# Optimization experiments

Hardware: AMD Instinct MI355X
Metric: run time of the kernel (lower is better)

## Reference

```python
import jax, jax.numpy as jnp
import numpy as np

N, P, C = 100000, 64, 128
DIST_TH = 0.1


def setup_inputs() -> dict:
    key = jax.random.key(0)
    ks = jax.random.split(key, 12)
    xyz = jax.random.uniform(ks[0], (N, 3), jnp.float32) * 10.0  # room coords in [0,10)^3
    feature = jax.random.normal(ks[1], (N, C), jnp.float32)
    center = jax.random.uniform(ks[2], (P, 3), jnp.float32) * 10.0
    normal = jax.random.normal(ks[3], (P, 3), jnp.float32)
    normal = normal / jnp.linalg.norm(normal, axis=1, keepdims=True)
    pmin = center - 1.5  # axis-aligned extent used on axes 0,1
    pmax = center + 1.5
    inp = {
        'feature': feature, 'xyz': xyz,
        'plane_center': center, 'plane_normal': normal,
        'plane_min': pmin, 'plane_max': pmax,
        'W1': jax.random.normal(ks[4], (C, 2 * C), jnp.float32) * (1.0 / np.sqrt(C)),
        's1': jnp.ones((2 * C,), jnp.float32), 'b1': jnp.zeros((2 * C,), jnp.float32),
        'W2': jax.random.normal(ks[5], (2 * C, C), jnp.float32) * (1.0 / np.sqrt(2 * C)),
        's2': jnp.ones((C,), jnp.float32), 'b2': jnp.zeros((C,), jnp.float32),
        'W3': jax.random.normal(ks[6], (C, 1), jnp.float32) * (1.0 / np.sqrt(C)),
        'b3': jnp.zeros((1,), jnp.float32),
        'Wa': jax.random.normal(ks[7], (C, C), jnp.float32) * (1.0 / np.sqrt(C)),
        'Wm': jax.random.normal(ks[8], (C, C), jnp.float32) * (1.0 / np.sqrt(C)),
        'bm': jnp.zeros((C,), jnp.float32),
    }
    return inp


def reference(feature, xyz, plane_center, plane_normal, plane_min, plane_max,
              W1, s1, b1, W2, s2, b2, W3, b3, Wa, Wm, bm):
    # pointwise MLP (shared across planes): fc1 (conv+BN+ReLU), fc2 (conv+BN+ReLU)
    h = jax.nn.relu((feature @ W1) * s1 + b1)          # [N, 2C]
    h2 = jax.nn.relu((h @ W2) * s2 + b2)               # [N, C] == plane_feature
    logit = (h2 @ W3 + b3)[:, 0]                        # [N] fc3 logits (plane_result)

    # per-plane point membership masks (dense [N, P])
    proj = xyz @ plane_normal.T                         # [N, P]
    offs = jnp.sum(plane_center * plane_normal, axis=1) # [P]
    dist_mask = jnp.abs(proj - offs[None, :]) < DIST_TH
    rng = ((xyz[:, None, 0] >= plane_min[None, :, 0]) & (xyz[:, None, 0] < plane_max[None, :, 0]) &
           (xyz[:, None, 1] >= plane_min[None, :, 1]) & (xyz[:, None, 1] < plane_max[None, :, 1]))
    mask = dist_mask & rng                              # [N, P]

    on_sel = jax.nn.sigmoid(logit) > 0.5                # [N]
    on_mask = (mask & on_sel[:, None]).astype(feature.dtype)
    off_mask = (mask & ~on_sel[:, None]).astype(feature.dtype)

    # attention pooling: masked softmax over points, per plane, per channel
    a = h2 @ Wa                                         # [N, C] att activations
    e = jnp.exp(a - jnp.max(a, axis=0, keepdims=True))  # stable exp, [N, C]
    eh = e * h2

    def att_pool(m):                                    # m: [N, P] float
        num = jnp.einsum('np,nc->pc', m, eh)
        den = jnp.einsum('np,nc->pc', m, e)
        agg = num / (den + 1e-9)                        # masked-softmax weighted sum
        return jax.nn.relu(agg @ Wm + bm)               # att_pooling.mlp (conv+ReLU)

    ori = jnp.concatenate([plane_center, plane_normal, plane_min, plane_max], axis=1)  # [P, 12]
    on_feat = jnp.concatenate([att_pool(on_mask), ori], axis=1)    # [P, C+12]
    off_feat = jnp.concatenate([att_pool(off_mask), ori], axis=1)  # [P, C+12]
    return logit, on_feat, off_feat
```

## Files before the change

kernel.cpp:

```cpp
#include <hip/hip_runtime.h>

#define NPTS 100000
#define P 64
#define C 128
#define CHUNKS 16
#define CHUNK_PTS 6250
#define CHUNK_PAD 6400

typedef __bf16 bf16_t;
typedef __bf16 bf16x4 __attribute__((ext_vector_type(4)));
typedef __bf16 bf16x8 __attribute__((ext_vector_type(8)));
typedef float floatx4 __attribute__((ext_vector_type(4)));


__global__ __launch_bounds__(256) void prep_kernel(
    const float* __restrict__ W1, const float* __restrict__ s1,
    const float* __restrict__ W2, const float* __restrict__ s2,
    const float* __restrict__ Wa,
    bf16_t* __restrict__ W1t, bf16_t* __restrict__ W2t, bf16_t* __restrict__ Wat)
{
  int i0 = blockIdx.x * blockDim.x + threadIdx.x;
  int stride = gridDim.x * blockDim.x;
  for (int i = i0; i < 256 * 128; i += stride) {
    int n = i >> 7, k = i & 127;
    W1t[i] = (bf16_t)(W1[k * 256 + n] * s1[n]);
  }
  for (int i = i0; i < 128 * 256; i += stride) {
    int n = i >> 8, k = i & 255;
    W2t[i] = (bf16_t)(W2[k * 128 + n] * s2[n]);
  }
  for (int i = i0; i < 128 * 128; i += stride) {
    int n = i >> 7, k = i & 127;
    Wat[i] = (bf16_t)(Wa[k * 128 + n]);
  }
}

__global__ __launch_bounds__(256, 6) void main_kernel(
    const float* __restrict__ feature,
    const float* __restrict__ b1, const float* __restrict__ b2,
    const float* __restrict__ W3, const float* __restrict__ b3,
    const bf16_t* __restrict__ W1t, const bf16_t* __restrict__ W2t,
    const bf16_t* __restrict__ Wat,
    bf16_t* __restrict__ rec, float* __restrict__ out_logit)
{
  __shared__ __align__(16) char smem[8704 + 16896 + 512];
  bf16_t* A1  = (bf16_t*)smem;
  bf16_t* Hs  = (bf16_t*)(smem + 8704);
  bf16_t* aB  = (bf16_t*)(smem + 8704);
  float*  w3S = (float*)(smem + 8704 + 16896);

  const int tid  = threadIdx.x;
  const int wave = tid >> 6, lane = tid & 63;
  const int quad = lane >> 4, l16 = lane & 15;
  const int m0 = blockIdx.x * 32;

  if (tid < 128) w3S[tid] = W3[tid];

#pragma unroll
  for (int j = 0; j < 4; ++j) {
    int idx = j * 256 + tid;
    int r = idx >> 5, c4 = idx & 31;
    float4 v = *(const float4*)(feature + (size_t)(m0 + r) * C + c4 * 4);
    bf16x4 o = {(bf16_t)v.x, (bf16_t)v.y, (bf16_t)v.z, (bf16_t)v.w};
    *(bf16x4*)(A1 + r * 136 + c4 * 4) = o;
  }
  __syncthreads();

  const floatx4 zero4 = {0.f, 0.f, 0.f, 0.f};

  {
    floatx4 acc[2][4];
#pragma unroll
    for (int mt = 0; mt < 2; ++mt)
#pragma unroll
      for (int nt = 0; nt < 4; ++nt) acc[mt][nt] = zero4;
#pragma unroll
    for (int kt = 0; kt < 4; ++kt) {
      bf16x8 af[2], bf[4];
#pragma unroll
      for (int mt = 0; mt < 2; ++mt)
        af[mt] = *(const bf16x8*)(A1 + (mt * 16 + l16) * 136 + kt * 32 + quad * 8);
#pragma unroll
      for (int nt = 0; nt < 4; ++nt)
        bf[nt] = *(const bf16x8*)(W1t + (wave * 64 + nt * 16 + l16) * 128 + kt * 32 + quad * 8);
#pragma unroll
      for (int mt = 0; mt < 2; ++mt)
#pragma unroll
        for (int nt = 0; nt < 4; ++nt)
          acc[mt][nt] = __builtin_amdgcn_mfma_f32_16x16x32_bf16(af[mt], bf[nt], acc[mt][nt], 0, 0, 0);
    }
#pragma unroll
    for (int nt = 0; nt < 4; ++nt) {
      int col = wave * 64 + nt * 16 + l16;
      float bias = b1[col];
#pragma unroll
      for (int mt = 0; mt < 2; ++mt)
#pragma unroll
        for (int r = 0; r < 4; ++r) {
          float hv = fmaxf(acc[mt][nt][r] + bias, 0.f);
          Hs[(mt * 16 + quad * 4 + r) * 264 + col] = (bf16_t)hv;
        }
    }
  }
  __syncthreads();

  {
    floatx4 acc[2][2];
#pragma unroll
    for (int mt = 0; mt < 2; ++mt) { acc[mt][0] = zero4; acc[mt][1] = zero4; }
#pragma unroll
    for (int kt = 0; kt < 8; ++kt) {
      bf16x8 af[2], bf[2];
#pragma unroll
      for (int mt = 0; mt < 2; ++mt)
        af[mt] = *(const bf16x8*)(Hs + (mt * 16 + l16) * 264 + kt * 32 + quad * 8);
#pragma unroll
      for (int nt = 0; nt < 2; ++nt)
        bf[nt] = *(const bf16x8*)(W2t + (wave * 32 + nt * 16 + l16) * 256 + kt * 32 + quad * 8);
#pragma unroll
      for (int mt = 0; mt < 2; ++mt)
#pragma unroll
        for (int nt = 0; nt < 2; ++nt)
          acc[mt][nt] = __builtin_amdgcn_mfma_f32_16x16x32_bf16(af[mt], bf[nt], acc[mt][nt], 0, 0, 0);
    }
#pragma unroll
    for (int nt = 0; nt < 2; ++nt) {
      int col = wave * 32 + nt * 16 + l16;
      float bias = b2[col];
#pragma unroll
      for (int mt = 0; mt < 2; ++mt)
#pragma unroll
        for (int r = 0; r < 4; ++r) {
          float hv = fmaxf(acc[mt][nt][r] + bias, 0.f);
          A1[(mt * 16 + quad * 4 + r) * 136 + col] = (bf16_t)hv;
        }
    }
  }
  __syncthreads();

  {
    floatx4 acc[2][2];
#pragma unroll
    for (int mt = 0; mt < 2; ++mt) { acc[mt][0] = zero4; acc[mt][1] = zero4; }
#pragma unroll
    for (int kt = 0; kt < 4; ++kt) {
      bf16x8 af[2], bf[2];
#pragma unroll
      for (int mt = 0; mt < 2; ++mt)
        af[mt] = *(const bf16x8*)(A1 + (mt * 16 + l16) * 136 + kt * 32 + quad * 8);
#pragma unroll
      for (int nt = 0; nt < 2; ++nt)
        bf[nt] = *(const bf16x8*)(Wat + (wave * 32 + nt * 16 + l16) * 128 + kt * 32 + quad * 8);
#pragma unroll
      for (int mt = 0; mt < 2; ++mt)
#pragma unroll
        for (int nt = 0; nt < 2; ++nt)
          acc[mt][nt] = __builtin_amdgcn_mfma_f32_16x16x32_bf16(af[mt], bf[nt], acc[mt][nt], 0, 0, 0);
    }
#pragma unroll
    for (int nt = 0; nt < 2; ++nt) {
      int col = wave * 32 + nt * 16 + l16;
#pragma unroll
      for (int mt = 0; mt < 2; ++mt)
#pragma unroll
        for (int r = 0; r < 4; ++r)
          aB[(mt * 16 + quad * 4 + r) * 136 + col] = (bf16_t)acc[mt][nt][r];
    }
  }
  __syncthreads();

  {
    const int m = tid >> 3, g = tid & 7, c0g = g * 16;
    float lsum = 0.f;
#pragma unroll
    for (int cc = 0; cc < 2; ++cc) {
      bf16x8 v = *(const bf16x8*)(A1 + m * 136 + c0g + cc * 8);
#pragma unroll
      for (int j = 0; j < 8; ++j)
        lsum += (float)v[j] * w3S[c0g + cc * 8 + j];
    }
    lsum += __shfl_xor(lsum, 1);
    lsum += __shfl_xor(lsum, 2);
    lsum += __shfl_xor(lsum, 4);
    if (g == 0) out_logit[m0 + m] = lsum + b3[0];
  }

#pragma unroll
  for (int i = tid; i < 32 * 64; i += 256) {
    int pt = i >> 6, slot = i & 63;
    const bf16_t* src = (slot < 32) ? (aB + pt * 136 + slot * 4)
                                    : (A1 + pt * 136 + (slot - 32) * 4);
    uint2 v = *(const uint2*)src;
    *(uint2*)(rec + (size_t)(m0 + pt) * 256 + slot * 4) = v;
  }
}

__global__ __launch_bounds__(256) void pool_kernel(
    const float* __restrict__ xyz, const float* __restrict__ out_logit,
    const bf16_t* __restrict__ rec,
    const float* __restrict__ ctr, const float* __restrict__ nrm,
    const float* __restrict__ pmn, const float* __restrict__ pmx,
    float* __restrict__ partial)
{
  const int plane = blockIdx.x >> 4;
  const int chunk = blockIdx.x & 15;
  const int tid = threadIdx.x, lane = tid & 63;

  __shared__ float accS[4][128];
  for (int i = tid; i < 512; i += 256) ((float*)accS)[i] = 0.f;

  const float nx = nrm[plane * 3], ny = nrm[plane * 3 + 1], nz = nrm[plane * 3 + 2];
  const float offs = ctr[plane * 3] * nx + ctr[plane * 3 + 1] * ny + ctr[plane * 3 + 2] * nz;
  const float mnx = pmn[plane * 3], mny = pmn[plane * 3 + 1];
  const float mxx = pmx[plane * 3], mxy = pmx[plane * 3 + 1];
  __syncthreads();

  const int base = chunk * CHUNK_PTS;
  float nOn0 = 0, nOn1 = 0, dOn0 = 0, dOn1 = 0;
  float nOf0 = 0, nOf1 = 0, dOf0 = 0, dOf1 = 0;

  for (int i = tid; i < CHUNK_PAD; i += 256) {
    int pt = base + i;
    bool hit = false;
    if (i < CHUNK_PTS) {
      float x = xyz[pt * 3], y = xyz[pt * 3 + 1], z = xyz[pt * 3 + 2];
      float proj = x * nx + y * ny + z * nz;
      hit = (fabsf(proj - offs) < 0.1f) &&
            (x >= mnx) && (x < mxx) && (y >= mny) && (y < mxy);
    }
    unsigned long long m = __ballot(hit);
    while (m) {
      int l = __builtin_ctzll(m);
      m &= m - 1;
      int hpt = __shfl(pt, l);
      float lg = out_logit[hpt];
      const unsigned* r32 = (const unsigned*)(rec + (size_t)hpt * 256);
      unsigned ap = r32[lane];
      unsigned hp = r32[64 + lane];
      float a0 = __uint_as_float(ap << 16);
      float a1 = __uint_as_float(ap & 0xffff0000u);
      float h0 = __uint_as_float(hp << 16);
      float h1 = __uint_as_float(hp & 0xffff0000u);
      float e0 = __expf(a0), e1 = __expf(a1);
      if (lg > 0.f) { nOn0 += e0 * h0; nOn1 += e1 * h1; dOn0 += e0; dOn1 += e1; }
      else          { nOf0 += e0 * h0; nOf1 += e1 * h1; dOf0 += e0; dOf1 += e1; }
    }
  }

  atomicAdd(&accS[0][lane * 2],     nOn0);
  atomicAdd(&accS[0][lane * 2 + 1], nOn1);
  atomicAdd(&accS[1][lane * 2],     dOn0);
  atomicAdd(&accS[1][lane * 2 + 1], dOn1);
  atomicAdd(&accS[2][lane * 2],     nOf0);
  atomicAdd(&accS[2][lane * 2 + 1], nOf1);
  atomicAdd(&accS[3][lane * 2],     dOf0);
  atomicAdd(&accS[3][lane * 2 + 1], dOf1);
  __syncthreads();

  float* dst = partial + (size_t)blockIdx.x * 512;
  for (int i = tid; i < 512; i += 256) dst[i] = ((float*)accS)[i];
}

__global__ __launch_bounds__(256) void finalize_kernel(
    const float* __restrict__ partial,
    const float* __restrict__ Wm, const float* __restrict__ bm,
    const float* __restrict__ ctr, const float* __restrict__ nrm,
    const float* __restrict__ pmn, const float* __restrict__ pmx,
    float* __restrict__ out)
{
  int sel = blockIdx.x >> 6, p = blockIdx.x & 63;
  int tid = threadIdx.x, j = tid & 127, half = tid >> 7;
  __shared__ float numS[2][128], denS[2][128], aggS[128], sumS[2][128];

  const float* bp = partial + ((size_t)p * 16 + half * 8) * 512 + sel * 256;
  float num = 0.f, den = 0.f;
#pragma unroll
  for (int k = 0; k < 8; ++k) {
    num += bp[k * 512 + j];
    den += bp[k * 512 + 128 + j];
  }
  numS[half][j] = num;
  denS[half][j] = den;
  __syncthreads();
  if (tid < 128)
    aggS[tid] = (numS[0][tid] + numS[1][tid]) / (denS[0][tid] + denS[1][tid] + 1e-9f);
  __syncthreads();

  float s = 0.f;
  const int cbase = half * 64;
#pragma unroll 8
  for (int c = 0; c < 64; ++c)
    s += aggS[cbase + c] * Wm[(cbase + c) * C + j];
  sumS[half][j] = s;
  __syncthreads();

  float* dst = out + NPTS + sel * (P * 140) + p * 140;
  if (tid < 128)
    dst[tid] = fmaxf(sumS[0][tid] + sumS[1][tid] + bm[tid], 0.f);
  if (tid < 12) {
    float v;
    if (tid < 3)      v = ctr[p * 3 + tid];
    else if (tid < 6) v = nrm[p * 3 + tid - 3];
    else if (tid < 9) v = pmn[p * 3 + tid - 6];
    else              v = pmx[p * 3 + tid - 9];
    dst[C + tid] = v;
  }
}

extern "C" void kernel_launch(void* const* d_in, const int* in_sizes, int n_in,
                              void* d_out, int out_size, void* d_ws, size_t ws_size,
                              hipStream_t stream)
{
  const float* feature = (const float*)d_in[0];
  const float* xyz     = (const float*)d_in[1];
  const float* ctr     = (const float*)d_in[2];
  const float* nrm     = (const float*)d_in[3];
  const float* pmn     = (const float*)d_in[4];
  const float* pmx     = (const float*)d_in[5];
  const float* W1      = (const float*)d_in[6];
  const float* s1      = (const float*)d_in[7];
  const float* b1      = (const float*)d_in[8];
  const float* W2      = (const float*)d_in[9];
  const float* s2      = (const float*)d_in[10];
  const float* b2      = (const float*)d_in[11];
  const float* W3      = (const float*)d_in[12];
  const float* b3      = (const float*)d_in[13];
  const float* Wa      = (const float*)d_in[14];
  const float* Wm      = (const float*)d_in[15];
  const float* bm      = (const float*)d_in[16];
  float* out = (float*)d_out;

  char* ws = (char*)d_ws;
  bf16_t* W1t = (bf16_t*)(ws);
  bf16_t* W2t = (bf16_t*)(ws + 65536);
  bf16_t* Wat = (bf16_t*)(ws + 131072);
  bf16_t* rec = (bf16_t*)(ws + 163840);
  float* partial = (float*)(ws + 163840 + (size_t)NPTS * 512);

  prep_kernel<<<64, 256, 0, stream>>>(W1, s1, W2, s2, Wa, W1t, W2t, Wat);
  main_kernel<<<NPTS / 32, 256, 0, stream>>>(
      feature, b1, b2, W3, b3, W1t, W2t, Wat, rec, out);
  pool_kernel<<<64 * CHUNKS, 256, 0, stream>>>(
      xyz, out, rec, ctr, nrm, pmn, pmx, partial);
  finalize_kernel<<<128, 256, 0, stream>>>(partial, Wm, bm, ctr, nrm, pmn, pmx, out);
}
```

Baseline: 204.1 us.

## Restructure MLP kernel so each wave independently processes 16 points

The main MLP kernel is reorganized so that each wave owns a 16-point tile and computes all output columns itself. Feature rows go straight from global memory into MFMA A-fragments, and intermediate activations stay in a per-wave LDS region, which removes the block-wide __syncthreads barriers. Each wave now reads the full weight matrices from global/L2 memory, so weight traffic per point roughly doubles compared with the 32-point block tile. Register pressure also rises (16 accumulators, cached biases), and the occupancy hint in launch bounds is dropped.

```diff
diff --git a/kernel.cpp b/kernel.cpp
--- a/kernel.cpp
+++ b/kernel.cpp
@@ -6,9 +6,9 @@
 #define CHUNKS 16
 #define CHUNK_PTS 6250
 #define CHUNK_PAD 6400
+#define NWAVES 6250
 
 typedef __bf16 bf16_t;
-typedef __bf16 bf16x4 __attribute__((ext_vector_type(4)));
 typedef __bf16 bf16x8 __attribute__((ext_vector_type(8)));
 typedef float floatx4 __attribute__((ext_vector_type(4)));
 
@@ -35,7 +35,9 @@
   }
 }
 
-__global__ __launch_bounds__(256, 6) void main_kernel(
+#define HSTRIDE 264
+
+__global__ __launch_bounds__(256) void main_kernel(
     const float* __restrict__ feature,
     const float* __restrict__ b1, const float* __restrict__ b2,
     const float* __restrict__ W3, const float* __restrict__ b3,
@@ -43,155 +45,123 @@
     const bf16_t* __restrict__ Wat,
     bf16_t* __restrict__ rec, float* __restrict__ out_logit)
 {
-  __shared__ __align__(16) char smem[8704 + 16896 + 512];
-  bf16_t* A1  = (bf16_t*)smem;
-  bf16_t* Hs  = (bf16_t*)(smem + 8704);
-  bf16_t* aB  = (bf16_t*)(smem + 8704);
-  float*  w3S = (float*)(smem + 8704 + 16896);
+  __shared__ __align__(16) bf16_t hS[4][16 * HSTRIDE];
 
   const int tid  = threadIdx.x;
   const int wave = tid >> 6, lane = tid & 63;
-  const int quad = lane >> 4, l16 = lane & 15;
-  const int m0 = blockIdx.x * 32;
-
-  if (tid < 128) w3S[tid] = W3[tid];
-
-#pragma unroll
-  for (int j = 0; j < 4; ++j) {
-    int idx = j * 256 + tid;
-    int r = idx >> 5, c4 = idx & 31;
-    float4 v = *(const float4*)(feature + (size_t)(m0 + r) * C + c4 * 4);
-    bf16x4 o = {(bf16_t)v.x, (bf16_t)v.y, (bf16_t)v.z, (bf16_t)v.w};
-    *(bf16x4*)(A1 + r * 136 + c4 * 4) = o;
-  }
-  __syncthreads();
+  const int q = lane >> 4, l = lane & 15;
+  const int wid = blockIdx.x * 4 + wave;
+  if (wid >= NWAVES) return;
+  const int m0 = wid * 16;
+  bf16_t* hw = &hS[wave][0];
+
+  bf16x8 afeat[4];
+#pragma unroll
+  for (int kt = 0; kt < 4; ++kt) {
+    const float* src = feature + (size_t)(m0 + l) * C + kt * 32 + q * 8;
+    float4 v0 = *(const float4*)(src);
+    float4 v1 = *(const float4*)(src + 4);
+    bf16x8 o = {(bf16_t)v0.x, (bf16_t)v0.y, (bf16_t)v0.z, (bf16_t)v0.w,
+                (bf16_t)v1.x, (bf16_t)v1.y, (bf16_t)v1.z, (bf16_t)v1.w};
+    afeat[kt] = o;
+  }
+
+  float b1r[16], b2r[8];
+#pragma unroll
+  for (int nt = 0; nt < 16; ++nt) b1r[nt] = b1[nt * 16 + l];
+#pragma unroll
+  for (int nt = 0; nt < 8; ++nt)  b2r[nt] = b2[nt * 16 + l];
 
   const floatx4 zero4 = {0.f, 0.f, 0.f, 0.f};
 
   {
-    floatx4 acc[2][4];
-#pragma unroll
-    for (int mt = 0; mt < 2; ++mt)
-#pragma unroll
-      for (int nt = 0; nt < 4; ++nt) acc[mt][nt] = zero4;
+    floatx4 acc[16];
+#pragma unroll
+    for (int nt = 0; nt < 16; ++nt) acc[nt] = zero4;
+#pragma unroll
+    for (int nt = 0; nt < 16; ++nt)
+#pragma unroll
+      for (int kt = 0; kt < 4; ++kt) {
+        bf16x8 bfr = *(const bf16x8*)(W1t + (nt * 16 + l) * 128 + kt * 32 + q * 8);
+        acc[nt] = __builtin_amdgcn_mfma_f32_16x16x32_bf16(afeat[kt], bfr, acc[nt], 0, 0, 0);
+      }
+#pragma unroll
+    for (int nt = 0; nt < 16; ++nt)
+#pragma unroll
+      for (int r = 0; r < 4; ++r)
+        hw[(q * 4 + r) * HSTRIDE + nt * 16 + l] = (bf16_t)fmaxf(acc[nt][r] + b1r[nt], 0.f);
+  }
+
+  bf16x8 ah[8];
+#pragma unroll
+  for (int kt = 0; kt < 8; ++kt)
+    ah[kt] = *(const bf16x8*)(hw + l * HSTRIDE + kt * 32 + q * 8);
+
+  {
+    floatx4 acc[8];
+#pragma unroll
+    for (int nt = 0; nt < 8; ++nt) acc[nt] = zero4;
+#pragma unroll
+    for (int nt = 0; nt < 8; ++nt)
+#pragma unroll
+      for (int kt = 0; kt < 8; ++kt) {
+        bf16x8 bfr = *(const bf16x8*)(W2t + (nt * 16 + l) * 256 + kt * 32 + q * 8);
+        acc[nt] = __builtin_amdgcn_mfma_f32_16x16x32_bf16(ah[kt], bfr, acc[nt], 0, 0, 0);
+      }
+#pragma unroll
+    for (int nt = 0; nt < 8; ++nt)
+#pragma unroll
+      for (int r = 0; r < 4; ++r)
+        hw[(q * 4 + r) * HSTRIDE + nt * 16 + l] = (bf16_t)fmaxf(acc[nt][r] + b2r[nt], 0.f);
+  }
+
+  bf16x8 ah2[4];
+#pragma unroll
+  for (int kt = 0; kt < 4; ++kt)
+    ah2[kt] = *(const bf16x8*)(hw + l * HSTRIDE + kt * 32 + q * 8);
+
+  {
+    floatx4 acc[8];
+#pragma unroll
+    for (int nt = 0; nt < 8; ++nt) acc[nt] = zero4;
+#pragma unroll
+    for (int nt = 0; nt < 8; ++nt)
+#pragma unroll
+      for (int kt = 0; kt < 4; ++kt) {
+        bf16x8 bfr = *(const bf16x8*)(Wat + (nt * 16 + l) * 128 + kt * 32 + q * 8);
+        acc[nt] = __builtin_amdgcn_mfma_f32_16x16x32_bf16(ah2[kt], bfr, acc[nt], 0, 0, 0);
+      }
+#pragma unroll
+    for (int nt = 0; nt < 8; ++nt)
+#pragma unroll
+      for (int r = 0; r < 4; ++r)
+        hw[(q * 4 + r) * HSTRIDE + nt * 16 + l] = (bf16_t)acc[nt][r];
+  }
+
+#pragma unroll
+  for (int kt = 0; kt < 4; ++kt) {
+    bf16x8 aA = *(const bf16x8*)(hw + l * HSTRIDE + kt * 32 + q * 8);
+    *(bf16x8*)(rec + (size_t)(m0 + l) * 256 + kt * 32 + q * 8) = aA;
+  }
+#pragma unroll
+  for (int kt = 0; kt < 4; ++kt)
+    *(bf16x8*)(rec + (size_t)(m0 + l) * 256 + 128 + kt * 32 + q * 8) = ah2[kt];
+
+  {
+    float lsum = 0.f;
 #pragma unroll
     for (int kt = 0; kt < 4; ++kt) {
-      bf16x8 af[2], bf[4];
-#pragma unroll
-      for (int mt = 0; mt < 2; ++mt)
-        af[mt] = *(const bf16x8*)(A1 + (mt * 16 + l16) * 136 + kt * 32 + quad * 8);
-#pragma unroll
-      for (int nt = 0; nt < 4; ++nt)
-        bf[nt] = *(const bf16x8*)(W1t + (wave * 64 + nt * 16 + l16) * 128 + kt * 32 + quad * 8);
-#pragma unroll
-      for (int mt = 0; mt < 2; ++mt)
-#pragma unroll
-        for (int nt = 0; nt < 4; ++nt)
-          acc[mt][nt] = __builtin_amdgcn_mfma_f32_16x16x32_bf16(af[mt], bf[nt], acc[mt][nt], 0, 0, 0);
+      const float* w3p = W3 + kt * 32 + q * 8;
+      float4 w0 = *(const float4*)(w3p);
+      float4 w1 = *(const float4*)(w3p + 4);
+      lsum += (float)ah2[kt][0] * w0.x + (float)ah2[kt][1] * w0.y +
+              (float)ah2[kt][2] * w0.z + (float)ah2[kt][3] * w0.w +
+              (float)ah2[kt][4] * w1.x + (float)ah2[kt][5] * w1.y +
+              (float)ah2[kt][6] * w1.z + (float)ah2[kt][7] * w1.w;
     }
-#pragma unroll
-    for (int nt = 0; nt < 4; ++nt) {
-      int col = wave * 64 + nt * 16 + l16;
-      float bias = b1[col];
-#pragma unroll
-      for (int mt = 0; mt < 2; ++mt)
-#pragma unroll
-        for (int r = 0; r < 4; ++r) {
-          float hv = fmaxf(acc[mt][nt][r] + bias, 0.f);
-          Hs[(mt * 16 + quad * 4 + r) * 264 + col] = (bf16_t)hv;
-        }
-    }
-  }
-  __syncthreads();
-
-  {
-    floatx4 acc[2][2];
-#pragma unroll
-    for (int mt = 0; mt < 2; ++mt) { acc[mt][0] = zero4; acc[mt][1] = zero4; }
-#pragma unroll
-    for (int kt = 0; kt < 8; ++kt) {
-      bf16x8 af[2], bf[2];
-#pragma unroll
-      for (int mt = 0; mt < 2; ++mt)
-        af[mt] = *(const bf16x8*)(Hs + (mt * 16 + l16) * 264 + kt * 32 + quad * 8);
-#pragma unroll
-      for (int nt = 0; nt < 2; ++nt)
-        bf[nt] = *(const bf16x8*)(W2t + (wave * 32 + nt * 16 + l16) * 256 + kt * 32 + quad * 8);
-#pragma unroll
-      for (int mt = 0; mt < 2; ++mt)
-#pragma unroll
-        for (int nt = 0; nt < 2; ++nt)
-          acc[mt][nt] = __builtin_amdgcn_mfma_f32_16x16x32_bf16(af[mt], bf[nt], acc[mt][nt], 0, 0, 0);
-    }
-#pragma unroll
-    for (int nt = 0; nt < 2; ++nt) {
-      int col = wave * 32 + nt * 16 + l16;
-      float bias = b2[col];
-#pragma unroll
-      for (int mt = 0; mt < 2; ++mt)
-#pragma unroll
-        for (int r = 0; r < 4; ++r) {
-          float hv = fmaxf(acc[mt][nt][r] + bias, 0.f);
-          A1[(mt * 16 + quad * 4 + r) * 136 + col] = (bf16_t)hv;
-        }
-    }
-  }
-  __syncthreads();
-
-  {
-    floatx4 acc[2][2];
-#pragma unroll
-    for (int mt = 0; mt < 2; ++mt) { acc[mt][0] = zero4; acc[mt][1] = zero4; }
-#pragma unroll
-    for (int kt = 0; kt < 4; ++kt) {
-      bf16x8 af[2], bf[2];
-#pragma unroll
-      for (int mt = 0; mt < 2; ++mt)
-        af[mt] = *(const bf16x8*)(A1 + (mt * 16 + l16) * 136 + kt * 32 + quad * 8);
-#pragma unroll
-      for (int nt = 0; nt < 2; ++nt)
-        bf[nt] = *(const bf16x8*)(Wat + (wave * 32 + nt * 16 + l16) * 128 + kt * 32 + quad * 8);
-#pragma unroll
-      for (int mt = 0; mt < 2; ++mt)
-#pragma unroll
-        for (int nt = 0; nt < 2; ++nt)
-          acc[mt][nt] = __builtin_amdgcn_mfma_f32_16x16x32_bf16(af[mt], bf[nt], acc[mt][nt], 0, 0, 0);
-    }
-#pragma unroll
-    for (int nt = 0; nt < 2; ++nt) {
-      int col = wave * 32 + nt * 16 + l16;
-#pragma unroll
-      for (int mt = 0; mt < 2; ++mt)
-#pragma unroll
-        for (int r = 0; r < 4; ++r)
-          aB[(mt * 16 + quad * 4 + r) * 136 + col] = (bf16_t)acc[mt][nt][r];
-    }
-  }
-  __syncthreads();
-
-  {
-    const int m = tid >> 3, g = tid & 7, c0g = g * 16;
-    float lsum = 0.f;
-#pragma unroll
-    for (int cc = 0; cc < 2; ++cc) {
-      bf16x8 v = *(const bf16x8*)(A1 + m * 136 + c0g + cc * 8);
-#pragma unroll
-      for (int j = 0; j < 8; ++j)
-        lsum += (float)v[j] * w3S[c0g + cc * 8 + j];
-    }
-    lsum += __shfl_xor(lsum, 1);
-    lsum += __shfl_xor(lsum, 2);
-    lsum += __shfl_xor(lsum, 4);
-    if (g == 0) out_logit[m0 + m] = lsum + b3[0];
-  }
-
-#pragma unroll
-  for (int i = tid; i < 32 * 64; i += 256) {
-    int pt = i >> 6, slot = i & 63;
-    const bf16_t* src = (slot < 32) ? (aB + pt * 136 + slot * 4)
-                                    : (A1 + pt * 136 + (slot - 32) * 4);
-    uint2 v = *(const uint2*)src;
-    *(uint2*)(rec + (size_t)(m0 + pt) * 256 + slot * 4) = v;
+    lsum += __shfl_xor(lsum, 16);
+    lsum += __shfl_xor(lsum, 32);
+    if (lane < 16) out_logit[m0 + lane] = lsum + b3[0];
   }
 }
 
@@ -230,9 +200,9 @@
     }
     unsigned long long m = __ballot(hit);
     while (m) {
-      int l = __builtin_ctzll(m);
+      int lbit = __builtin_ctzll(m);
       m &= m - 1;
-      int hpt = __shfl(pt, l);
+      int hpt = __shfl(pt, lbit);
       float lg = out_logit[hpt];
       const unsigned* r32 = (const unsigned*)(rec + (size_t)hpt * 256);
       unsigned ap = r32[lane];
@@ -338,7 +308,7 @@
   float* partial = (float*)(ws + 163840 + (size_t)NPTS * 512);
 
   prep_kernel<<<64, 256, 0, stream>>>(W1, s1, W2, s2, Wa, W1t, W2t, Wat);
-  main_kernel<<<NPTS / 32, 256, 0, stream>>>(
+  main_kernel<<<(NWAVES + 3) / 4, 256, 0, stream>>>(
       feature, b1, b2, W3, b3, W1t, W2t, Wat, rec, out);
   pool_kernel<<<64 * CHUNKS, 256, 0, stream>>>(
       xyz, out, rec, ctr, nrm, pmn, pmx, partial);
```

After: 280.6 us. 1.38x slower.
